# Optimization experiments

Hardware: AMD Instinct MI355X
Metric: run time of the kernel (lower is better)

Reference implementation:

```python
import jax, jax.numpy as jnp
import numpy as np

B, IN, OUT, LAT = 8192, 256, 256, 128

def setup_inputs() -> dict:
    key = jax.random.key(0)
    ks = jax.random.split(key, 6)
    s = 0.05
    return {
        "x": jax.random.normal(ks[0], (B, IN), dtype=jnp.float32),
        "latent": jax.random.normal(ks[1], (B, LAT), dtype=jnp.float32),
        "Ww": jax.random.normal(ks[2], (LAT, IN * OUT), dtype=jnp.float32) * s,
        "bw": jax.random.normal(ks[3], (IN * OUT,), dtype=jnp.float32) * s,
        "Wb": jax.random.normal(ks[4], (LAT, OUT), dtype=jnp.float32) * s,
        "bb": jax.random.normal(ks[5], (OUT,), dtype=jnp.float32) * s,
    }

def reference(x, latent, Ww, bw, Wb, bb):
    lead = x.shape[:-1]
    x2 = x.reshape(-1, x.shape[-1])            # [B, in]
    l2 = latent.reshape(-1, latent.shape[-1])  # [B, lat]
    # per-sample weight: [B, in, out]
    weight = (l2 @ Ww + bw).reshape(-1, IN, OUT)
    # per-sample bias: [B, out]
    bias = l2 @ Wb + bb
    out = jnp.einsum('bi,bio->bo', x2, weight) + bias
    return out.reshape(*lead, OUT)
```

## Files before the change

kernel.cpp:

```cpp
#include <hip/hip_runtime.h>
#include <cstdint>
#include <cstddef>

#define BATCH  8192
#define IN_N   256
#define OUT_N  256
#define LAT_N  128
#define SLABS  129
#define KT     (SLABS * IN_N)
#define KT16   (KT / 16)
#define SPLITK 4

typedef _Float16 h8 __attribute__((ext_vector_type(8)));
typedef _Float16 h4 __attribute__((ext_vector_type(4)));
typedef _Float16 h2 __attribute__((ext_vector_type(2)));
typedef float    f16v __attribute__((ext_vector_type(16)));
typedef float    f4v  __attribute__((ext_vector_type(4)));

#define AS1 __attribute__((address_space(1)))
#define AS3 __attribute__((address_space(3)))
#define WAITVM0 asm volatile("s_waitcnt vmcnt(0)" ::: "memory")
#define WAITVM2 asm volatile("s_waitcnt vmcnt(2)" ::: "memory")
#define WAITVM4 asm volatile("s_waitcnt vmcnt(4)" ::: "memory")

#define WS_BP    0
#define WS_XH    16908288
#define WS_LT    21102592
#define WS_PARTS 23216128

#define PR_T1   516
#define PR_L1   580
#define PR_X1   1604
#define PR_O1   1608
#define PR_B1   2632
__global__ void k_prep(const float* __restrict__ Ww, const float* __restrict__ bw,
                       const float* __restrict__ x,  const float* __restrict__ latent,
                       const float* __restrict__ Wb, const float* __restrict__ bb,
                       _Float16* __restrict__ Bp, _Float16* __restrict__ Xh,
                       _Float16* __restrict__ LT, float* __restrict__ part0) {
    __shared__ _Float16 smemh[16512];
    const int bid = blockIdx.x;
    const int t   = threadIdx.x;

    if (bid < PR_T1) {
        _Float16* tile = smemh;
        const int k0 = bid * 64;
#pragma unroll
        for (int j = 0; j < 16; ++j) {
            int idx = j * 256 + t;
            int row = idx >> 6, col = (idx & 63) * 4;
            int k = k0 + row;
            const float* src = (k < LAT_N * IN_N)
                             ? Ww + (size_t)k * 256 + col
                             : bw + (size_t)(k - LAT_N * IN_N) * 256 + col;
            float4 v = *(const float4*)src;
            h4 o;
            o[0] = (_Float16)v.x; o[1] = (_Float16)v.y;
            o[2] = (_Float16)v.z; o[3] = (_Float16)v.w;
            *(h4*)(tile + row * 256 + col) = o;
        }
        __syncthreads();
        const int tl = t & 31;
#pragma unroll
        for (int j = 0; j < 4; ++j) {
            int stid = j * 8 + (t >> 5);
            int kt_l = stid >> 3, nt = stid & 7;
            int kt16 = bid * 4 + kt_l;
            _Float16* dst = Bp + ((size_t)(nt * KT16 + kt16) * 64) * 8;
#pragma unroll
            for (int kh = 0; kh < 2; ++kh) {
                h8 v;
#pragma unroll
                for (int h = 0; h < 8; ++h)
                    v[h] = tile[(kt_l * 16 + kh * 8 + h) * 256 + nt * 32 + tl];
                *(h8*)(dst + (size_t)(kh * 32 + tl) * 8) = v;
            }
        }
    } else if (bid < PR_L1) {
        _Float16* t2 = smemh;
        const int b0 = (bid - PR_T1) * 128;
#pragma unroll
        for (int j = 0; j < 16; ++j) {
            int idx = j * 256 + t;
            int b = idx >> 5, l = (idx & 31) * 4;
            float4 v = *(const float4*)(latent + (size_t)(b0 + b) * 128 + l);
            t2[(l + 0) * 129 + b] = (_Float16)v.x;
            t2[(l + 1) * 129 + b] = (_Float16)v.y;
            t2[(l + 2) * 129 + b] = (_Float16)v.z;
            t2[(l + 3) * 129 + b] = (_Float16)v.w;
        }
        __syncthreads();
#pragma unroll
        for (int j = 0; j < 32; ++j) {
            int idx = j * 256 + t;
            int l = idx >> 6, bb2 = (idx & 63) * 2;
            h2 w;
            w[0] = t2[l * 129 + bb2];
            w[1] = t2[l * 129 + bb2 + 1];
            *(h2*)(LT + (size_t)l * BATCH + b0 + bb2) = w;
        }
    } else if (bid < PR_X1) {
        const int cb = bid - PR_L1;
        int i = (cb * 256 + t) * 8;
        float4 v0 = *(const float4*)(x + i);
        float4 v1 = *(const float4*)(x + i + 4);
        h8 o;
        o[0] = (_Float16)v0.x; o[1] = (_Float16)v0.y;
        o[2] = (_Float16)v0.z; o[3] = (_Float16)v0.w;
        o[4] = (_Float16)v1.x; o[5] = (_Float16)v1.y;
        o[6] = (_Float16)v1.z; o[7] = (_Float16)v1.w;
        *(h8*)(Xh + i) = o;
    } else if (bid < PR_O1) {
        const int ob = bid - PR_X1;
        int base = ob * 2048 + t * 8;
        h8 o;
#pragma unroll
        for (int h = 0; h < 8; ++h) o[h] = (_Float16)1.0f;
        *(h8*)(LT + (size_t)LAT_N * BATCH + base) = o;
    } else {
        float* lat = (float*)smemh;
        const int b0 = (bid - PR_O1) * 8;
#pragma unroll
        for (int j = 0; j < 4; ++j) {
            int idx = t + 256 * j;
            int rr = idx >> 7, l = idx & 127;
            lat[rr * 128 + l] = latent[(size_t)(b0 + rr) * 128 + l];
        }
        __syncthreads();
        const int o = t;
        float acc[8];
        float bbv = bb[o];
#pragma unroll
        for (int rr = 0; rr < 8; ++rr) acc[rr] = bbv;
        for (int l = 0; l < 128; ++l) {
            float w = Wb[l * 256 + o];
#pragma unroll
            for (int rr = 0; rr < 8; ++rr) acc[rr] += lat[rr * 128 + l] * w;
        }
#pragma unroll
        for (int rr = 0; rr < 8; ++rr) part0[(size_t)(b0 + rr) * 256 + o] = acc[rr];
    }
}

__global__ __launch_bounds__(512, 1) void k_gemm(const _Float16* __restrict__ Bp,
                                                 const _Float16* __restrict__ Xh,
                                                 const _Float16* __restrict__ LT,
                                                 float* __restrict__ parts) {
    __shared__ __align__(16) _Float16 Bs[4 * 8192];

    const int bid   = blockIdx.x;
    const int ks    = bid & 3;
    const int m_blk = bid >> 2;
    const int m0    = m_blk * 128;
    const int slab0 = (ks == 0) ? 0 : 33 + 32 * (ks - 1);
    const int nslab = (ks == 0) ? 33 : 32;

    const int tid = threadIdx.x, wid = tid >> 6, lane = tid & 63;
    const int l32 = lane & 31, khalf = lane >> 5;
    const int wm = wid >> 2, wn = wid & 3;
    const int mrow0 = m0 + wm * 64 + l32;
    const int mrow1 = mrow0 + 32;

    h8 xv0[16], xv1[16];
    const _Float16* xp0 = Xh + (size_t)mrow0 * IN_N + khalf * 8;
    const _Float16* xp1 = Xh + (size_t)mrow1 * IN_N + khalf * 8;
#pragma unroll
    for (int k = 0; k < 16; ++k) {
        xv0[k] = *(const h8*)(xp0 + k * 16);
        xv1[k] = *(const h8*)(xp1 + k * 16);
    }

    const _Float16* ltp = LT + (size_t)slab0 * BATCH;
    _Float16 sc0 = ltp[mrow0], sc1 = ltp[mrow1];

    const int chunk0 = wid * 2;
    const char* Bgb = (const char*)Bp;

#define STAGE(bufidx, ktg)                                                                 \
    _Pragma("unroll")                                                                      \
    for (int i_ = 0; i_ < 2; ++i_) {                                                       \
        const int c_   = chunk0 + i_;                                                      \
        const int ktl_ = c_ >> 3, nt_ = c_ & 7;                                            \
        const char* g_ = Bgb + (((size_t)(nt_ * KT16 + (ktg) + ktl_)) << 10) + (lane << 4);\
        _Float16* l_ = Bs + (bufidx) * 8192 + c_ * 512;                                    \
        __builtin_amdgcn_global_load_lds((const AS1 void*)g_, (AS3 void*)l_, 16, 0, 0);    \
    }

#define DSREAD(d0, d1, d2, d3, bufc)                                                       \
    {                                                                                      \
        const _Float16* bb_ = Bs + (bufc) * 8192 + wn * 1024 + (lane << 3);                \
        d0 = *(const h8*)(bb_);                                                            \
        d1 = *(const h8*)(bb_ + 512);                                                      \
        d2 = *(const h8*)(bb_ + 4096);                                                     \
        d3 = *(const h8*)(bb_ + 4608);                                                     \
    }

    f16v acc00, acc01, acc10, acc11;
#pragma unroll
    for (int r = 0; r < 16; ++r) { acc00[r] = 0.f; acc01[r] = 0.f; acc10[r] = 0.f; acc11[r] = 0.f; }

#define KSTEPR(sl)                                                                         \
    {                                                                                      \
        const int kx0 = (((sl) * 2 + 0) & 15), kx1 = (((sl) * 2 + 1) & 15);                \
        h8 a00 = xv0[kx0] * s80;                                                           \
        h8 a10 = xv1[kx0] * s81;                                                           \
        __builtin_amdgcn_s_setprio(1);                                                     \
        acc00 = __builtin_amdgcn_mfma_f32_32x32x16_f16(a00, c0, acc00, 0, 0, 0);           \
        acc01 = __builtin_amdgcn_mfma_f32_32x32x16_f16(a00, c1, acc01, 0, 0, 0);           \
        acc10 = __builtin_amdgcn_mfma_f32_32x32x16_f16(a10, c0, acc10, 0, 0, 0);           \
        acc11 = __builtin_amdgcn_mfma_f32_32x32x16_f16(a10, c1, acc11, 0, 0, 0);           \
        __builtin_amdgcn_s_setprio(0);                                                     \
        h8 a01 = xv0[kx1] * s80;                                                           \
        h8 a11 = xv1[kx1] * s81;                                                           \
        __builtin_amdgcn_s_setprio(1);                                                     \
        acc00 = __builtin_amdgcn_mfma_f32_32x32x16_f16(a01, c2, acc00, 0, 0, 0);           \
        acc01 = __builtin_amdgcn_mfma_f32_32x32x16_f16(a01, c3, acc01, 0, 0, 0);           \
        acc10 = __builtin_amdgcn_mfma_f32_32x32x16_f16(a11, c2, acc10, 0, 0, 0);           \
        acc11 = __builtin_amdgcn_mfma_f32_32x32x16_f16(a11, c3, acc11, 0, 0, 0);           \
        __builtin_amdgcn_s_setprio(0);                                                     \
    }

    const int kb = slab0 * 16;
    h8 c0, c1, c2, c3, n0, n1, n2, n3;

    STAGE(0, kb + 0);
    STAGE(1, kb + 2);
    STAGE(2, kb + 4);
    WAITVM2;
    __builtin_amdgcn_s_barrier();
    asm volatile("" ::: "memory");
    DSREAD(c0, c1, c2, c3, 0);

    for (int s0 = 0; s0 < nslab - 1; ++s0) {
        _Float16 sn0 = ltp[(size_t)(s0 + 1) * BATCH + mrow0];
        _Float16 sn1 = ltp[(size_t)(s0 + 1) * BATCH + mrow1];
        h8 s80, s81;
#pragma unroll
        for (int h = 0; h < 8; ++h) { s80[h] = sc0; s81[h] = sc1; }
        const int ktg0 = kb + s0 * 16;
#pragma unroll
        for (int sl = 0; sl < 8; ++sl) {
            STAGE((sl + 3) & 3, ktg0 + (sl + 3) * 2);
            DSREAD(n0, n1, n2, n3, (sl + 1) & 3);
            KSTEPR(sl);
            if (sl == 0) WAITVM4; else WAITVM2;
            __builtin_amdgcn_s_barrier();
            asm volatile("" ::: "memory");
            c0 = n0; c1 = n1; c2 = n2; c3 = n3;
        }
        sc0 = sn0; sc1 = sn1;
    }

    {
        h8 s80, s81;
#pragma unroll
        for (int h = 0; h < 8; ++h) { s80[h] = sc0; s81[h] = sc1; }
        const int ktg0 = kb + (nslab - 1) * 16;
#pragma unroll
        for (int sl = 0; sl < 8; ++sl) {
            if (sl <= 4) STAGE((sl + 3) & 3, ktg0 + (sl + 3) * 2);
            if (sl < 7) DSREAD(n0, n1, n2, n3, (sl + 1) & 3);
            KSTEPR(sl);
            if (sl <= 4) WAITVM2;
            else if (sl == 5) WAITVM0;
            if (sl <= 5) {
                __builtin_amdgcn_s_barrier();
                asm volatile("" ::: "memory");
            }
            if (sl < 7) { c0 = n0; c1 = n1; c2 = n2; c3 = n3; }
        }
    }

    float* dst = parts + (size_t)ks * ((size_t)BATCH * OUT_N);
    const int rowb0 = m0 + wm * 64;
#define EPI(rowb, u, accv)                                                                 \
    {                                                                                      \
        int col = wn * 64 + (u) * 32 + l32;                                                \
        _Pragma("unroll")                                                                  \
        for (int r = 0; r < 16; ++r) {                                                     \
            int row = (rowb) + (r & 3) + 8 * (r >> 2) + 4 * khalf;                         \
            size_t off = (size_t)row * OUT_N + col;                                        \
            if (ks == 0) dst[off] += accv[r];                                              \
            else         dst[off] = accv[r];                                               \
        }                                                                                  \
    }
    EPI(rowb0,      0, acc00); EPI(rowb0,      1, acc01);
    EPI(rowb0 + 32, 0, acc10); EPI(rowb0 + 32, 1, acc11);
#undef EPI
#undef KSTEPR
#undef DSREAD
#undef STAGE
}

__global__ void k_reduce(const float* __restrict__ parts, float* __restrict__ out) {
    int i = (blockIdx.x * 256 + threadIdx.x) * 4;
    f4v s = *(const f4v*)(parts + i);
    s += *(const f4v*)(parts + 2097152 + i);
    s += *(const f4v*)(parts + 2 * 2097152 + i);
    s += *(const f4v*)(parts + 3 * 2097152 + i);
    *(f4v*)(out + i) = s;
}

extern "C" void kernel_launch(void* const* d_in, const int* in_sizes, int n_in,
                              void* d_out, int out_size, void* d_ws, size_t ws_size,
                              hipStream_t stream) {
    const float* x      = (const float*)d_in[0];
    const float* latent = (const float*)d_in[1];
    const float* Ww     = (const float*)d_in[2];
    const float* bw     = (const float*)d_in[3];
    const float* Wb     = (const float*)d_in[4];
    const float* bb     = (const float*)d_in[5];

    char* ws = (char*)d_ws;
    _Float16* Bp    = (_Float16*)(ws + WS_BP);
    _Float16* Xh    = (_Float16*)(ws + WS_XH);
    _Float16* LT    = (_Float16*)(ws + WS_LT);
    float*    parts = (float*)(ws + WS_PARTS);
    float*    out   = (float*)d_out;

    k_prep<<<PR_B1, 256, 0, stream>>>(Ww, bw, x, latent, Wb, bb, Bp, Xh, LT, parts);
    k_gemm<<<256, 512, 0, stream>>>(Bp, Xh, LT, parts);
    k_reduce<<<2048, 256, 0, stream>>>(parts, out);
}
```

Baseline: 255.8 us.

## Give each wave a private LDS ring for B tiles and drop block barriers

Each wave now stages its own copy of the B fragments it needs into a private LDS region, instead of sharing cooperatively staged tiles across the block. This removes every s_barrier from the main loop, so only per-wave vmcnt waits guard the LDS reads. In exchange each wave issues twice as many global-to-LDS loads, B data is fetched redundantly by the two waves sharing a column group, and LDS use per block doubles.

After: 276.5 us. 1.08x slower.

```diff
diff --git a/kernel.cpp b/kernel.cpp
--- a/kernel.cpp
+++ b/kernel.cpp
@@ -19,9 +19,11 @@
 
 #define AS1 __attribute__((address_space(1)))
 #define AS3 __attribute__((address_space(3)))
-#define WAITVM0 asm volatile("s_waitcnt vmcnt(0)" ::: "memory")
-#define WAITVM2 asm volatile("s_waitcnt vmcnt(2)" ::: "memory")
-#define WAITVM4 asm volatile("s_waitcnt vmcnt(4)" ::: "memory")
+#define WAITVM0  asm volatile("s_waitcnt vmcnt(0)" ::: "memory")
+#define WAITVM4  asm volatile("s_waitcnt vmcnt(4)" ::: "memory")
+#define WAITVM8  asm volatile("s_waitcnt vmcnt(8)" ::: "memory")
+#define WAITVM10 asm volatile("s_waitcnt vmcnt(10)" ::: "memory")
+#define MEMFENCE asm volatile("" ::: "memory")
 
 #define WS_BP    0
 #define WS_XH    16908288
@@ -146,7 +148,7 @@
                                                  const _Float16* __restrict__ Xh,
                                                  const _Float16* __restrict__ LT,
                                                  float* __restrict__ parts) {
-    __shared__ __align__(16) _Float16 Bs[4 * 8192];
+    __shared__ __align__(16) _Float16 Bs[8 * 4 * 2048];
 
     const int bid   = blockIdx.x;
     const int ks    = bid & 3;
@@ -161,6 +163,8 @@
     const int mrow0 = m0 + wm * 64 + l32;
     const int mrow1 = mrow0 + 32;
 
+    _Float16* myBs = Bs + wid * 8192;
+
     h8 xv0[16], xv1[16];
     const _Float16* xp0 = Xh + (size_t)mrow0 * IN_N + khalf * 8;
     const _Float16* xp1 = Xh + (size_t)mrow1 * IN_N + khalf * 8;
@@ -173,26 +177,25 @@
     const _Float16* ltp = LT + (size_t)slab0 * BATCH;
     _Float16 sc0 = ltp[mrow0], sc1 = ltp[mrow1];
 
-    const int chunk0 = wid * 2;
     const char* Bgb = (const char*)Bp;
 
 #define STAGE(bufidx, ktg)                                                                 \
     _Pragma("unroll")                                                                      \
-    for (int i_ = 0; i_ < 2; ++i_) {                                                       \
-        const int c_   = chunk0 + i_;                                                      \
-        const int ktl_ = c_ >> 3, nt_ = c_ & 7;                                            \
+    for (int f_ = 0; f_ < 4; ++f_) {                                                       \
+        const int ktl_ = f_ >> 1, ntl_ = f_ & 1;                                           \
+        const int nt_  = 2 * wn + ntl_;                                                    \
         const char* g_ = Bgb + (((size_t)(nt_ * KT16 + (ktg) + ktl_)) << 10) + (lane << 4);\
-        _Float16* l_ = Bs + (bufidx) * 8192 + c_ * 512;                                    \
+        _Float16* l_ = myBs + (bufidx) * 2048 + f_ * 512;                                  \
         __builtin_amdgcn_global_load_lds((const AS1 void*)g_, (AS3 void*)l_, 16, 0, 0);    \
     }
 
 #define DSREAD(d0, d1, d2, d3, bufc)                                                       \
     {                                                                                      \
-        const _Float16* bb_ = Bs + (bufc) * 8192 + wn * 1024 + (lane << 3);                \
+        const _Float16* bb_ = myBs + (bufc) * 2048 + (lane << 3);                          \
         d0 = *(const h8*)(bb_);                                                            \
         d1 = *(const h8*)(bb_ + 512);                                                      \
-        d2 = *(const h8*)(bb_ + 4096);                                                     \
-        d3 = *(const h8*)(bb_ + 4608);                                                     \
+        d2 = *(const h8*)(bb_ + 1024);                                                     \
+        d3 = *(const h8*)(bb_ + 1536);                                                     \
     }
 
     f16v acc00, acc01, acc10, acc11;
@@ -223,12 +226,11 @@
     const int kb = slab0 * 16;
     h8 c0, c1, c2, c3, n0, n1, n2, n3;
 
+    MEMFENCE;
     STAGE(0, kb + 0);
     STAGE(1, kb + 2);
     STAGE(2, kb + 4);
-    WAITVM2;
-    __builtin_amdgcn_s_barrier();
-    asm volatile("" ::: "memory");
+    WAITVM8;
     DSREAD(c0, c1, c2, c3, 0);
 
     for (int s0 = 0; s0 < nslab - 1; ++s0) {
@@ -241,11 +243,9 @@
 #pragma unroll
         for (int sl = 0; sl < 8; ++sl) {
             STAGE((sl + 3) & 3, ktg0 + (sl + 3) * 2);
+            if (sl == 0) WAITVM10; else WAITVM8;
             DSREAD(n0, n1, n2, n3, (sl + 1) & 3);
             KSTEPR(sl);
-            if (sl == 0) WAITVM4; else WAITVM2;
-            __builtin_amdgcn_s_barrier();
-            asm volatile("" ::: "memory");
             c0 = n0; c1 = n1; c2 = n2; c3 = n3;
         }
         sc0 = sn0; sc1 = sn1;
@@ -259,14 +259,11 @@
 #pragma unroll
         for (int sl = 0; sl < 8; ++sl) {
             if (sl <= 4) STAGE((sl + 3) & 3, ktg0 + (sl + 3) * 2);
+            if (sl <= 4) { WAITVM8; }
+            else if (sl == 5) { WAITVM4; }
+            else if (sl == 6) { WAITVM0; }
             if (sl < 7) DSREAD(n0, n1, n2, n3, (sl + 1) & 3);
             KSTEPR(sl);
-            if (sl <= 4) WAITVM2;
-            else if (sl == 5) WAITVM0;
-            if (sl <= 5) {
-                __builtin_amdgcn_s_barrier();
-                asm volatile("" ::: "memory");
-            }
             if (sl < 7) { c0 = n0; c1 = n1; c2 = n2; c3 = n3; }
         }
     }
```
